# Kernel tuning notes

Measured on AMD Instinct MI355X. Metric: run time of the kernel, lower is better.

## Reference

```python
import jax, jax.numpy as jnp
import numpy as np

B, P, N, E, F, L = 64, 512, 512, 128, 512, 6
SQRT_E = 11.313708498984761
CLIP = 10.0
EPS = 1e-5

def _inorm(x, w, b):
    # InstanceNorm1d over node dim (axis=1) per (batch, channel); x: [B,N,E]
    mu = x.mean(axis=1, keepdims=True)
    var = x.var(axis=1, keepdims=True)
    return (x - mu) * jax.lax.rsqrt(var + EPS) * w + b

def setup_inputs():
    key = jax.random.key(0)
    ks = jax.random.split(key, 24)
    nrm = lambda k, shp, s=0.05: jax.random.normal(k, shp, dtype=jnp.float32) * s
    inp = {}
    inp['data'] = jax.random.uniform(ks[0], (B, N, 2), dtype=jnp.float32)
    inp['dist'] = -jax.random.uniform(ks[1], (B, N, N), dtype=jnp.float32)      # negative dist
    inp['cur_dist'] = -jax.random.uniform(ks[2], (B, P, N), dtype=jnp.float32)
    inp['capacity'] = jax.random.uniform(ks[3], (B, P), dtype=jnp.float32)
    inp['ninf_mask'] = jnp.zeros((B, P, N), jnp.float32)
    inp['log_scale'] = jnp.array([1.0], jnp.float32)
    # encoder params (Linear weights stored [in,out], i.e. torch weight transposed)
    inp['emb_W'] = nrm(ks[4], (2, E), 0.5); inp['emb_b'] = jnp.zeros((E,), jnp.float32)
    inp['Wq'] = nrm(ks[5], (L, E, E)); inp['Wk'] = nrm(ks[6], (L, E, E)); inp['Wv'] = nrm(ks[7], (L, E, E))
    inp['aft_alpha'] = jnp.ones((L,), jnp.float32)
    inp['n1_w'] = jnp.ones((L, E), jnp.float32); inp['n1_b'] = jnp.zeros((L, E), jnp.float32)
    inp['ff_W1'] = nrm(ks[8], (L, E, F)); inp['ff_b1'] = jnp.zeros((L, F), jnp.float32)
    inp['ff_W2'] = nrm(ks[9], (L, F, E)); inp['ff_b2'] = jnp.zeros((L, E), jnp.float32)
    inp['n2_w'] = jnp.ones((L, E), jnp.float32); inp['n2_b'] = jnp.zeros((L, E), jnp.float32)
    # decoder params
    inp['dWq'] = nrm(ks[10], (E + 1, E)); inp['dWk'] = nrm(ks[11], (E, E)); inp['dWv'] = nrm(ks[12], (E, E))
    inp['dec_aft_alpha'] = jnp.array([1.0], jnp.float32)
    inp['probs_alpha'] = jnp.array([1.0], jnp.float32)
    return inp

def reference(data, dist, cur_dist, capacity, ninf_mask, log_scale,
              emb_W, emb_b, Wq, Wk, Wv, aft_alpha, n1_w, n1_b,
              ff_W1, ff_b1, ff_W2, ff_b2, n2_w, n2_b,
              dWq, dWk, dWv, dec_aft_alpha, probs_alpha):
    ls = log_scale[0]
    # ---- encoder: stacked AFT layers ----
    x = data @ emb_W + emb_b                                   # [B,N,E]
    for l in range(L):
        q = x @ Wq[l]; k = x @ Wk[l]; v = x @ Wv[l]
        ad = jnp.exp(ls * aft_alpha[l] * dist)                 # [B,N,N]
        ek = jnp.exp(k)
        weighted = (ad @ (ek * v)) / (ad @ ek)                 # [B,N,E]
        out = jax.nn.sigmoid(q) * weighted
        h = _inorm(x + out, n1_w[l], n1_b[l])
        ff = jax.nn.relu(h @ ff_W1[l] + ff_b1[l]) @ ff_W2[l] + ff_b2[l]
        x = _inorm(h + ff, n2_w[l], n2_b[l])
    enc = x                                                    # [B,N,E]
    # ---- decoder ----
    k = enc @ dWk; v = enc @ dWv
    gmean = enc.mean(axis=1, keepdims=True)                    # [B,1,E]
    gmp = jnp.broadcast_to(gmean, (enc.shape[0], capacity.shape[1], enc.shape[2]))
    q = jnp.concatenate([gmp, capacity[:, :, None]], axis=2) @ dWq   # [B,P,E]
    ad = jnp.exp(ls * dec_aft_alpha[0] * cur_dist + ninf_mask)       # [B,P,N]
    ek = jnp.exp(k)
    weighted = (ad @ (ek * v)) / (ad @ ek)                     # [B,P,E]
    aft = jax.nn.sigmoid(q) * weighted
    score = jnp.einsum('bpe,bne->bpn', aft, enc) / SQRT_E
    score = score + ls * probs_alpha[0] * cur_dist
    score = CLIP * jnp.tanh(score) + ninf_mask
    return jax.nn.softmax(score, axis=2)                       # [B,P,N]
```

## Files before the change

### kernel.cpp

```cpp
#include <hip/hip_runtime.h>
#include <math.h>

#define B_ 64
#define N_ 512
#define P_ 512
#define E_ 128
#define F_ 512
#define L_ 6
#define SQRT_E_INV 0.08838834764831843f

typedef unsigned short u16;
typedef __attribute__((ext_vector_type(8))) short bf8;
typedef __attribute__((ext_vector_type(16))) float f16v;

__device__ inline u16 bf16r(float f) {
    unsigned u = __float_as_uint(f);
    u += 0x7fffu + ((u >> 16) & 1u);
    return (u16)(u >> 16);
}
__device__ inline float bf2f(u16 h) { return __uint_as_float((unsigned)h << 16); }

#define MFMA(a, b, c) __builtin_amdgcn_mfma_f32_32x32x16_bf16(a, b, c, 0, 0, 0)

struct Q3 {
    const u16 *A0, *A1;
    const u16 *qh, *ql, *vh, *vl, *kh, *kl;
    u16 *sq16, *y2t;
};

__launch_bounds__(256, 2) __global__ void qvk3_k(Q3 p)
{
    const int tid = threadIdx.x;
    const int lane = tid & 63, wv = tid >> 6;
    const int wm = wv & 1, wn = wv >> 1;
    const int ln = lane & 31, hk = lane >> 5;
    const int row0 = blockIdx.x * 64;

    __shared__ __align__(16) u16 As[2][64][40];
    __shared__ __align__(16) u16 Bs[6][128][40];

    f16v aq[2], av[2], ak[2];
#pragma unroll
    for (int nt = 0; nt < 2; ++nt)
#pragma unroll
        for (int q = 0; q < 16; ++q) { aq[nt][q] = 0.f; av[nt][q] = 0.f; ak[nt][q] = 0.f; }

    const int r = tid >> 2, kq = tid & 3;
    for (int k0 = 0; k0 < 128; k0 += 32) {
        size_t ga = (size_t)(row0 + r) * 128 + k0 + kq * 8;
        *(uint4*)&As[0][r][kq * 8] = *(const uint4*)(p.A0 + ga);
        *(uint4*)&As[1][r][kq * 8] = *(const uint4*)(p.A1 + ga);
#pragma unroll
        for (int i = 0; i < 2; ++i) {
            int s = tid + i * 256;
            int rb2 = s >> 2, q = s & 3;
            size_t gb = (size_t)rb2 * 128 + k0 + q * 8;
            *(uint4*)&Bs[0][rb2][q * 8] = *(const uint4*)(p.qh + gb);
            *(uint4*)&Bs[1][rb2][q * 8] = *(const uint4*)(p.ql + gb);
            *(uint4*)&Bs[2][rb2][q * 8] = *(const uint4*)(p.vh + gb);
            *(uint4*)&Bs[3][rb2][q * 8] = *(const uint4*)(p.vl + gb);
            *(uint4*)&Bs[4][rb2][q * 8] = *(const uint4*)(p.kh + gb);
            *(uint4*)&Bs[5][rb2][q * 8] = *(const uint4*)(p.kl + gb);
        }
        __syncthreads();
#pragma unroll
        for (int s = 0; s < 2; ++s) {
            bf8 ah = *(const bf8*)&As[0][wm * 32 + ln][s * 16 + hk * 8];
            bf8 al = *(const bf8*)&As[1][wm * 32 + ln][s * 16 + hk * 8];
#pragma unroll
            for (int nt = 0; nt < 2; ++nt) {
                const int br = wn * 64 + nt * 32 + ln, sc = s * 16 + hk * 8;
                bf8 bqh = *(const bf8*)&Bs[0][br][sc];
                bf8 bql = *(const bf8*)&Bs[1][br][sc];
                bf8 bvh = *(const bf8*)&Bs[2][br][sc];
                bf8 bvl = *(const bf8*)&Bs[3][br][sc];
                bf8 bkh = *(const bf8*)&Bs[4][br][sc];
                bf8 bkl = *(const bf8*)&Bs[5][br][sc];
                aq[nt] = MFMA(ah, bqh, aq[nt]);
                aq[nt] = MFMA(ah, bql, aq[nt]);
                aq[nt] = MFMA(al, bqh, aq[nt]);
                av[nt] = MFMA(ah, bvh, av[nt]);
                av[nt] = MFMA(ah, bvl, av[nt]);
                av[nt] = MFMA(al, bvh, av[nt]);
                ak[nt] = MFMA(ah, bkh, ak[nt]);
                ak[nt] = MFMA(ah, bkl, ak[nt]);
                ak[nt] = MFMA(al, bkh, ak[nt]);
            }
        }
        __syncthreads();
    }

#pragma unroll
    for (int nt = 0; nt < 2; ++nt) {
        int gn = wn * 64 + nt * 32 + ln;
#pragma unroll
        for (int g = 0; g < 4; ++g) {
            int rb = row0 + wm * 32 + g * 8 + hk * 4;
            int bb = rb >> 9, nb = rb & 511;
            u16 pe[4], pv[4];
#pragma unroll
            for (int rr = 0; rr < 4; ++rr) {
                float vq = aq[nt][g * 4 + rr];
                p.sq16[(size_t)(rb + rr) * 128 + gn] =
                    bf16r(1.f / (1.f + __expf(-vq)));
                u16 hv = bf16r(av[nt][g * 4 + rr]);
                u16 he = bf16r(__expf(ak[nt][g * 4 + rr]));
                pe[rr] = he;
                pv[rr] = bf16r(bf2f(hv) * bf2f(he));
            }
            uint2 ue, uv;
            ue.x = pe[0] | ((unsigned)pe[1] << 16);
            ue.y = pe[2] | ((unsigned)pe[3] << 16);
            uv.x = pv[0] | ((unsigned)pv[1] << 16);
            uv.y = pv[2] | ((unsigned)pv[3] << 16);
            *(uint2*)(p.y2t + (size_t)bb * 131072 + (size_t)gn * 512 + nb) = uv;
            *(uint2*)(p.y2t + (size_t)bb * 131072 + (size_t)(128 + gn) * 512 + nb) = ue;
        }
    }
}

struct QV {
    const u16 *A0, *A1;
    const u16 *vh, *vl, *kh, *kl;
    u16* y2t;
};

__launch_bounds__(256, 3) __global__ void qvk_vk_k(QV p)
{
    const int tid = threadIdx.x;
    const int lane = tid & 63, wv = tid >> 6;
    const int wm = wv & 1, wn = wv >> 1;
    const int ln = lane & 31, hk = lane >> 5;
    const int row0 = blockIdx.x * 64;

    __shared__ __align__(16) u16 As[2][64][40];
    __shared__ __align__(16) u16 Bs[4][128][40];

    f16v av[2], ak[2];
#pragma unroll
    for (int nt = 0; nt < 2; ++nt)
#pragma unroll
        for (int q = 0; q < 16; ++q) { av[nt][q] = 0.f; ak[nt][q] = 0.f; }

    const int r = tid >> 2, kq = tid & 3;
    for (int k0 = 0; k0 < 128; k0 += 32) {
        size_t ga = (size_t)(row0 + r) * 128 + k0 + kq * 8;
        *(uint4*)&As[0][r][kq * 8] = *(const uint4*)(p.A0 + ga);
        *(uint4*)&As[1][r][kq * 8] = *(const uint4*)(p.A1 + ga);
#pragma unroll
        for (int i = 0; i < 2; ++i) {
            int s = tid + i * 256;
            int rb2 = s >> 2, q = s & 3;
            size_t gb = (size_t)rb2 * 128 + k0 + q * 8;
            *(uint4*)&Bs[0][rb2][q * 8] = *(const uint4*)(p.vh + gb);
            *(uint4*)&Bs[1][rb2][q * 8] = *(const uint4*)(p.vl + gb);
            *(uint4*)&Bs[2][rb2][q * 8] = *(const uint4*)(p.kh + gb);
            *(uint4*)&Bs[3][rb2][q * 8] = *(const uint4*)(p.kl + gb);
        }
        __syncthreads();
#pragma unroll
        for (int s = 0; s < 2; ++s) {
            bf8 ah = *(const bf8*)&As[0][wm * 32 + ln][s * 16 + hk * 8];
            bf8 al = *(const bf8*)&As[1][wm * 32 + ln][s * 16 + hk * 8];
#pragma unroll
            for (int nt = 0; nt < 2; ++nt) {
                const int br = wn * 64 + nt * 32 + ln, sc = s * 16 + hk * 8;
                bf8 bvh = *(const bf8*)&Bs[0][br][sc];
                bf8 bvl = *(const bf8*)&Bs[1][br][sc];
                bf8 bkh = *(const bf8*)&Bs[2][br][sc];
                bf8 bkl = *(const bf8*)&Bs[3][br][sc];
                av[nt] = MFMA(ah, bvh, av[nt]);
                av[nt] = MFMA(ah, bvl, av[nt]);
                av[nt] = MFMA(al, bvh, av[nt]);
                ak[nt] = MFMA(ah, bkh, ak[nt]);
                ak[nt] = MFMA(ah, bkl, ak[nt]);
                ak[nt] = MFMA(al, bkh, ak[nt]);
            }
        }
        __syncthreads();
    }

#pragma unroll
    for (int nt = 0; nt < 2; ++nt) {
        int gn = wn * 64 + nt * 32 + ln;
#pragma unroll
        for (int g = 0; g < 4; ++g) {
            int rb = row0 + wm * 32 + g * 8 + hk * 4;
            int bb = rb >> 9, nb = rb & 511;
            u16 pe[4], pv[4];
#pragma unroll
            for (int rr = 0; rr < 4; ++rr) {
                u16 hv = bf16r(av[nt][g * 4 + rr]);
                u16 he = bf16r(__expf(ak[nt][g * 4 + rr]));
                pe[rr] = he;
                pv[rr] = bf16r(bf2f(hv) * bf2f(he));
            }
            uint2 ue, uv;
            ue.x = pe[0] | ((unsigned)pe[1] << 16);
            ue.y = pe[2] | ((unsigned)pe[3] << 16);
            uv.x = pv[0] | ((unsigned)pv[1] << 16);
            uv.y = pv[2] | ((unsigned)pv[3] << 16);
            *(uint2*)(p.y2t + (size_t)bb * 131072 + (size_t)gn * 512 + nb) = uv;
            *(uint2*)(p.y2t + (size_t)bb * 131072 + (size_t)(128 + gn) * 512 + nb) = ue;
        }
    }
}

struct AP2 {
    const float *A0, *A1;
    const u16 *B0, *sq;
    u16 *gh, *gl;
    const float *s1, *s2; int s2i;
};

template <int OPA, int SG>
__launch_bounds__(256, 3) __global__ void aft2_k(AP2 p)
{
    const int tid = threadIdx.x;
    const int lane = tid & 63, wv = tid >> 6;
    const int wm = wv & 1, wn = wv >> 1;
    const int ln = lane & 31, hk = lane >> 5;

    const int id = blockIdx.x;
    const int xcd = id & 7, slot = id >> 3;
    const int bz = xcd * 8 + (slot >> 3);
    const int row0 = (slot & 7) * 64;

    __shared__ __align__(16) u16 As[2][64][40];
    __shared__ __align__(16) u16 Bs[2][256][40];

    f16v acc[4];
#pragma unroll
    for (int j = 0; j < 4; ++j)
#pragma unroll
        for (int q = 0; q < 16; ++q) acc[j][q] = 0.f;

    const float ascale = p.s1[0] * p.s2[p.s2i];
    const float* Af = p.A0 + (size_t)bz * 262144 + (size_t)row0 * 512;
    const float* Mf = (OPA == 2)
        ? (p.A1 + (size_t)bz * 262144 + (size_t)row0 * 512) : (const float*)0;
    const u16* Bb = p.B0 + (size_t)bz * 131072;

    const int r = tid >> 2, kq = tid & 3;
    float fa[8], fm[8];
    uint4 vb[4];

#define AFT_LOAD(K0)                                                          \
    {                                                                         \
        size_t ga = (size_t)r * 512 + (K0) + kq * 8;                          \
        *(float4*)&fa[0] = *(const float4*)(Af + ga);                         \
        *(float4*)&fa[4] = *(const float4*)(Af + ga + 4);                     \
        if (OPA == 2) {                                                       \
            *(float4*)&fm[0] = *(const float4*)(Mf + ga);                     \
            *(float4*)&fm[4] = *(const float4*)(Mf + ga + 4);                 \
        }                                                                     \
        size_t gb = (size_t)tid * 512 + (K0);                                 \
        _Pragma("unroll") for (int q = 0; q < 4; ++q)                         \
            vb[q] = *(const uint4*)(Bb + gb + q * 8);                         \
    }

#define AFT_WRITE(BUF)                                                        \
    {                                                                         \
        float f[8];                                                           \
        _Pragma("unroll") for (int j = 0; j < 8; ++j) {                       \
            float t = (OPA == 2) ? fmaf(ascale, fa[j], fm[j]) : ascale * fa[j]; \
            f[j] = __expf(t);                                                 \
        }                                                                     \
        uint4 pk;                                                             \
        pk.x = bf16r(f[0]) | ((unsigned)bf16r(f[1]) << 16);                   \
        pk.y = bf16r(f[2]) | ((unsigned)bf16r(f[3]) << 16);                   \
        pk.z = bf16r(f[4]) | ((unsigned)bf16r(f[5]) << 16);                   \
        pk.w = bf16r(f[6]) | ((unsigned)bf16r(f[7]) << 16);                   \
        *(uint4*)&As[BUF][r][kq * 8] = pk;                                    \
        _Pragma("unroll") for (int q = 0; q < 4; ++q)                         \
            *(uint4*)&Bs[BUF][tid][q * 8] = vb[q];                            \
    }

#define AFT_COMPUTE(BUF)                                                      \
    {                                                                         \
        _Pragma("unroll") for (int s = 0; s < 2; ++s) {                       \
            bf8 ah = *(const bf8*)&As[BUF][wm * 32 + ln][s * 16 + hk * 8];    \
            _Pragma("unroll") for (int j = 0; j < 4; ++j) {                   \
                int br = ((j >> 1) << 7) + wn * 64 + ((j & 1) << 5) + ln;     \
                bf8 bh = *(const bf8*)&Bs[BUF][br][s * 16 + hk * 8];          \
                acc[j] = MFMA(ah, bh, acc[j]);                                \
            }                                                                 \
        }                                                                     \
    }

    AFT_LOAD(0);
    AFT_WRITE(0);
    __syncthreads();

    int cur = 0;
    for (int k0 = 32; k0 < 512; k0 += 32) {
        AFT_LOAD(k0);
        AFT_COMPUTE(cur);
        AFT_WRITE(cur ^ 1);
        __syncthreads();
        cur ^= 1;
    }
    AFT_COMPUTE(cur);

#undef AFT_LOAD
#undef AFT_WRITE
#undef AFT_COMPUTE

    const u16* sqb = SG ? (p.sq + (size_t)bz * 65536) : (const u16*)0;
    u16* ghb = p.gh + (size_t)bz * 65536;
    u16* glb = p.gl + (size_t)bz * 65536;
#pragma unroll
    for (int j = 0; j < 2; ++j) {
        int e = wn * 64 + j * 32 + ln;
#pragma unroll
        for (int g = 0; g < 4; ++g) {
#pragma unroll
            for (int rr = 0; rr < 4; ++rr) {
                int row = row0 + wm * 32 + g * 8 + hk * 4 + rr;
                float num = acc[j][g * 4 + rr];
                float den = acc[j + 2][g * 4 + rr];
                float pv = num / den;
                if (SG) pv *= bf2f(sqb[(size_t)row * 128 + e]);
                u16 hi = bf16r(pv);
                ghb[(size_t)row * 128 + e] = hi;
                glb[(size_t)row * 128 + e] = bf16r(pv - bf2f(hi));
            }
        }
    }
}

struct F12 {
    const u16 *A0, *A1;
    const u16 *w1h, *w1l;
    const u16 *w2h, *w2l;
    const float *b1, *b2;
    float* of;
};

__launch_bounds__(512, 2) __global__ void ffn12_k(F12 p)
{
    const int tid = threadIdx.x;
    const int lane = tid & 63, wv = tid >> 6;
    const int wm = wv & 1, wn = wv >> 1;
    const int ln = lane & 31, hk = lane >> 5;
    const int row0 = blockIdx.x * 64;

    __shared__ __align__(16) u16 Bs[2][128][136];
    __shared__ __align__(16) u16 ff1c[4][64][136];

    bf8 ar0[8], ar1[8];
    {
        const size_t arow = (size_t)(row0 + wm * 32 + ln) * 128;
#pragma unroll
        for (int s = 0; s < 8; ++s) {
            ar0[s] = *(const bf8*)(p.A0 + arow + s * 16 + hk * 8);
            ar1[s] = *(const bf8*)(p.A1 + arow + s * 16 + hk * 8);
        }
    }

    const int lcol = wn * 32 + ln;

    for (int ct = 0; ct < 4; ++ct) {
#pragma unroll
        for (int i = 0; i < 4; ++i) {
            int idx = tid + i * 512;
            int col = idx >> 4, q = idx & 15;
            size_t gb = (size_t)(ct * 128 + col) * 128 + q * 8;
            *(uint4*)&Bs[0][col][q * 8] = *(const uint4*)(p.w1h + gb);
            *(uint4*)&Bs[1][col][q * 8] = *(const uint4*)(p.w1l + gb);
        }
        __syncthreads();

        f16v a0, a1, a2;
#pragma unroll
        for (int q = 0; q < 16; ++q) { a0[q] = 0.f; a1[q] = 0.f; a2[q] = 0.f; }
#pragma unroll
        for (int s = 0; s < 8; ++s) {
            bf8 bh = *(const bf8*)&Bs[0][lcol][s * 16 + hk * 8];
            bf8 bl = *(const bf8*)&Bs[1][lcol][s * 16 + hk * 8];
            a0 = MFMA(ar0[s], bh, a0);
            a1 = MFMA(ar0[s], bl, a1);
            a2 = MFMA(ar1[s], bh, a2);
        }
        __syncthreads();

        float bv = p.b1[ct * 128 + lcol];
#pragma unroll
        for (int g = 0; g < 4; ++g) {
#pragma unroll
            for (int rr = 0; rr < 4; ++rr) {
                int lr = wm * 32 + g * 8 + hk * 4 + rr;
                float v = a0[g * 4 + rr] + a1[g * 4 + rr] + a2[g * 4 + rr] + bv;
                ff1c[ct][lr][lcol] = bf16r(fmaxf(v, 0.f));
            }
        }
    }
    __syncthreads();

    f16v c0, c1;
#pragma unroll
    for (int q = 0; q < 16; ++q) { c0[q] = 0.f; c1[q] = 0.f; }
    for (int kc = 0; kc < 4; ++kc) {
#pragma unroll
        for (int i = 0; i < 4; ++i) {
            int idx = tid + i * 512;
            int col = idx >> 4, q = idx & 15;
            size_t gb = (size_t)col * 512 + kc * 128 + q * 8;
            *(uint4*)&Bs[0][col][q * 8] = *(const uint4*)(p.w2h + gb);
            *(uint4*)&Bs[1][col][q * 8] = *(const uint4*)(p.w2l + gb);
        }
        __syncthreads();
#pragma unroll
        for (int s = 0; s < 8; ++s) {
            bf8 af = *(const bf8*)&ff1c[kc][wm * 32 + ln][s * 16 + hk * 8];
            bf8 bh = *(const bf8*)&Bs[0][lcol][s * 16 + hk * 8];
            bf8 bl = *(const bf8*)&Bs[1][lcol][s * 16 + hk * 8];
            c0 = MFMA(af, bh, c0);
            c1 = MFMA(af, bl, c1);
        }
        __syncthreads();
    }

    float bv = p.b2[lcol];
#pragma unroll
    for (int g = 0; g < 4; ++g) {
#pragma unroll
        for (int rr = 0; rr < 4; ++rr) {
            int rb = row0 + wm * 32 + g * 8 + hk * 4 + rr;
            p.of[(size_t)rb * 128 + lcol] = c0[g * 4 + rr] + c1[g * 4 + rr] + bv;
        }
    }
}

struct SP2 {
    const u16 *A0, *A1, *B0, *B1;
    float* out;
    const float *cd, *cm;
    const float *s1, *s2;
};

__launch_bounds__(256, 2) __global__ void score_sm_k(SP2 p)
{
    const int tid = threadIdx.x;
    const int lane = tid & 63, wv = tid >> 6;
    const int wm = wv & 1, wn = wv >> 1;
    const int ln = lane & 31, hk = lane >> 5;

    const int id = blockIdx.x;
    const int xcd = id & 7, s_ = id >> 3;
    const int bz = xcd * 8 + (s_ & 7);
    const int row0 = (s_ >> 3) * 64;

    __shared__ __align__(16) u16 As[2][64][136];
    __shared__ __align__(16) u16 Bs[2][128][72];
    __shared__ float rs[2][64];

#pragma unroll
    for (int i = 0; i < 8; ++i) {
        int idx = tid + i * 256;
        int pl = idx >> 10, rem = idx & 1023;
        int row = rem >> 4, q = rem & 15;
        const u16* src = pl ? p.A1 : p.A0;
        *(uint4*)&As[pl][row][q * 8] =
            *(const uint4*)(src + ((size_t)bz * 512 + row0 + row) * 128 + q * 8);
    }

    const float sp = p.s1[0] * p.s2[0];
    f16v accs[4][2];
    float rsum[16];
#pragma unroll
    for (int i = 0; i < 16; ++i) rsum[i] = 0.f;

#pragma unroll
    for (int ct = 0; ct < 4; ++ct) {
#pragma unroll
        for (int nt = 0; nt < 2; ++nt)
#pragma unroll
            for (int q = 0; q < 16; ++q) accs[ct][nt][q] = 0.f;

        for (int kc = 0; kc < 128; kc += 64) {
#pragma unroll
            for (int i = 0; i < 8; ++i) {
                int idx = tid + i * 256;
                int pl = idx >> 10, rem = idx & 1023;
                int row = rem >> 3, q = rem & 7;
                const u16* src = pl ? p.B1 : p.B0;
                *(uint4*)&Bs[pl][row][q * 8] =
                    *(const uint4*)(src + ((size_t)bz * 512 + ct * 128 + row) * 128
                                    + kc + q * 8);
            }
            __syncthreads();
#pragma unroll
            for (int s = 0; s < 4; ++s) {
                bf8 ah = *(const bf8*)&As[0][wm * 32 + ln][kc + s * 16 + hk * 8];
                bf8 al = *(const bf8*)&As[1][wm * 32 + ln][kc + s * 16 + hk * 8];
#pragma unroll
                for (int nt = 0; nt < 2; ++nt) {
                    bf8 bh = *(const bf8*)&Bs[0][wn * 64 + nt * 32 + ln][s * 16 + hk * 8];
                    bf8 bl = *(const bf8*)&Bs[1][wn * 64 + nt * 32 + ln][s * 16 + hk * 8];
                    accs[ct][nt] = MFMA(ah, bh, accs[ct][nt]);
                    accs[ct][nt] = MFMA(ah, bl, accs[ct][nt]);
                    accs[ct][nt] = MFMA(al, bh, accs[ct][nt]);
                }
            }
            __syncthreads();
        }

#pragma unroll
        for (int nt = 0; nt < 2; ++nt) {
            int gn = ct * 128 + wn * 64 + nt * 32 + ln;
#pragma unroll
            for (int g = 0; g < 4; ++g) {
#pragma unroll
                for (int rr = 0; rr < 4; ++rr) {
                    int grow = row0 + wm * 32 + g * 8 + hk * 4 + rr;
                    size_t ix = (size_t)bz * 262144 + (size_t)grow * 512 + gn;
                    float sc = fmaf(accs[ct][nt][g * 4 + rr], SQRT_E_INV,
                                    sp * p.cd[ix]);
                    float e2 = __expf(2.f * sc);
                    float th = 1.f - 2.f / (e2 + 1.f);
                    float ev = __expf(10.f * th + p.cm[ix]);
                    accs[ct][nt][g * 4 + rr] = ev;
                    rsum[g * 4 + rr] += ev;
                }
            }
        }
    }

#pragma unroll
    for (int i = 0; i < 16; ++i) {
#pragma unroll
        for (int o = 1; o < 32; o <<= 1) rsum[i] += __shfl_xor(rsum[i], o);
    }
    __syncthreads();
    if (ln == 0) {
#pragma unroll
        for (int i = 0; i < 16; ++i) {
            int lr = wm * 32 + (i >> 2) * 8 + hk * 4 + (i & 3);
            rs[wn][lr] = rsum[i];
        }
    }
    __syncthreads();
    float invr[16];
#pragma unroll
    for (int i = 0; i < 16; ++i) {
        int lr = wm * 32 + (i >> 2) * 8 + hk * 4 + (i & 3);
        invr[i] = 1.f / (rs[0][lr] + rs[1][lr]);
    }

#pragma unroll
    for (int ct = 0; ct < 4; ++ct)
#pragma unroll
        for (int nt = 0; nt < 2; ++nt) {
            int gn = ct * 128 + wn * 64 + nt * 32 + ln;
#pragma unroll
            for (int g = 0; g < 4; ++g)
#pragma unroll
                for (int rr = 0; rr < 4; ++rr) {
                    int grow = row0 + wm * 32 + g * 8 + hk * 4 + rr;
                    size_t ix = (size_t)bz * 262144 + (size_t)grow * 512 + gn;
                    p.out[ix] = accs[ct][nt][g * 4 + rr] * invr[g * 4 + rr];
                }
        }
}

template <int MODE>
__launch_bounds__(256) __global__ void inorm_k(
    const u16* __restrict__ ah, const u16* __restrict__ al,
    const u16* __restrict__ g0, const u16* __restrict__ g1,
    const float* __restrict__ f1,
    const float* __restrict__ nw, const float* __restrict__ nbv,
    u16* __restrict__ oh, u16* __restrict__ ol)
{
    const int bb = blockIdx.x, e0 = blockIdx.y * 16;
    const int tid = threadIdx.x, el = tid & 3, no = tid >> 2;
    const size_t base = (size_t)bb * N_ * E_ + e0 + el * 4;

    float4 vals[8];
    float s1x = 0, s1y = 0, s1z = 0, s1w = 0;
    float s2x = 0, s2y = 0, s2z = 0, s2w = 0;
#pragma unroll
    for (int i = 0; i < 8; ++i) {
        int n = no * 8 + i;
        size_t ad = base + (size_t)n * E_;
        uint2 h2 = *(const uint2*)(ah + ad);
        uint2 l2 = *(const uint2*)(al + ad);
        float x0 = bf2f((u16)h2.x) + bf2f((u16)l2.x);
        float x1 = bf2f((u16)(h2.x >> 16)) + bf2f((u16)(l2.x >> 16));
        float x2 = bf2f((u16)h2.y) + bf2f((u16)l2.y);
        float x3 = bf2f((u16)(h2.y >> 16)) + bf2f((u16)(l2.y >> 16));
        float4 v;
        if (MODE == 1) {
            uint2 a2 = *(const uint2*)(g0 + ad);
            uint2 b2 = *(const uint2*)(g1 + ad);
            v.x = x0 + bf2f((u16)a2.x) + bf2f((u16)b2.x);
            v.y = x1 + bf2f((u16)(a2.x >> 16)) + bf2f((u16)(b2.x >> 16));
            v.z = x2 + bf2f((u16)a2.y) + bf2f((u16)b2.y);
            v.w = x3 + bf2f((u16)(a2.y >> 16)) + bf2f((u16)(b2.y >> 16));
        } else {
            float4 ff = *(const float4*)(f1 + ad);
            v.x = x0 + ff.x; v.y = x1 + ff.y; v.z = x2 + ff.z; v.w = x3 + ff.w;
        }
        vals[i] = v;
        s1x += v.x; s1y += v.y; s1z += v.z; s1w += v.w;
        s2x = fmaf(v.x, v.x, s2x); s2y = fmaf(v.y, v.y, s2y);
        s2z = fmaf(v.z, v.z, s2z); s2w = fmaf(v.w, v.w, s2w);
    }

    __shared__ float4 r1[256], r2[256];
    r1[tid] = make_float4(s1x, s1y, s1z, s1w);
    r2[tid] = make_float4(s2x, s2y, s2z, s2w);
    __syncthreads();
    for (int s = 128; s >= 4; s >>= 1) {
        if (tid < s) {
            float4 u = r1[tid], w = r1[tid + s];
            r1[tid] = make_float4(u.x + w.x, u.y + w.y, u.z + w.z, u.w + w.w);
            float4 pq = r2[tid], q = r2[tid + s];
            r2[tid] = make_float4(pq.x + q.x, pq.y + q.y, pq.z + q.z, pq.w + q.w);
        }
        __syncthreads();
    }
    __shared__ float4 mu_s[4], rs_s[4];
    if (tid < 4) {
        float4 m = r1[tid], q = r2[tid];
        m.x *= (1.f / N_); m.y *= (1.f / N_); m.z *= (1.f / N_); m.w *= (1.f / N_);
        q.x *= (1.f / N_); q.y *= (1.f / N_); q.z *= (1.f / N_); q.w *= (1.f / N_);
        float4 rsq;
        rsq.x = rsqrtf(q.x - m.x * m.x + 1e-5f);
        rsq.y = rsqrtf(q.y - m.y * m.y + 1e-5f);
        rsq.z = rsqrtf(q.z - m.z * m.z + 1e-5f);
        rsq.w = rsqrtf(q.w - m.w * m.w + 1e-5f);
        mu_s[tid] = m; rs_s[tid] = rsq;
    }
    __syncthreads();
    float4 mu = mu_s[el], rsq = rs_s[el];
    float4 w4 = *(const float4*)(nw + e0 + el * 4);
    float4 b4 = *(const float4*)(nbv + e0 + el * 4);
#pragma unroll
    for (int i = 0; i < 8; ++i) {
        size_t ad = base + (size_t)(no * 8 + i) * E_;
        float4 v = vals[i];
        v.x = fmaf((v.x - mu.x) * rsq.x, w4.x, b4.x);
        v.y = fmaf((v.y - mu.y) * rsq.y, w4.y, b4.y);
        v.z = fmaf((v.z - mu.z) * rsq.z, w4.z, b4.z);
        v.w = fmaf((v.w - mu.w) * rsq.w, w4.w, b4.w);
        u16 h0 = bf16r(v.x), h1 = bf16r(v.y), h2v = bf16r(v.z), h3 = bf16r(v.w);
        u16 l0 = bf16r(v.x - bf2f(h0)), l1 = bf16r(v.y - bf2f(h1));
        u16 l2v = bf16r(v.z - bf2f(h2v)), l3 = bf16r(v.w - bf2f(h3));
        uint2 ph, pl;
        ph.x = h0 | ((unsigned)h1 << 16); ph.y = h2v | ((unsigned)h3 << 16);
        pl.x = l0 | ((unsigned)l1 << 16); pl.y = l2v | ((unsigned)l3 << 16);
        *(uint2*)(oh + ad) = ph;
        *(uint2*)(ol + ad) = pl;
    }
}

__global__ void wprep_k(const float* __restrict__ W, u16* __restrict__ Th,
                        u16* __restrict__ Tl, int K, int N)
{
    const int z = blockIdx.z;
    const float* Wz = W + (size_t)z * K * N;
    u16* Hh = Th + (size_t)z * K * N;
    u16* Hl = Tl + (size_t)z * K * N;
    __shared__ float t[32][33];
    const int j = threadIdx.x & 31, i0 = threadIdx.x >> 5;
    const int k0 = blockIdx.x * 32, n0 = blockIdx.y * 32;
    for (int i = i0; i < 32; i += 8)
        t[i][j] = Wz[(size_t)(k0 + i) * N + n0 + j];
    __syncthreads();
    for (int i = i0; i < 32; i += 8) {
        float v = t[j][i];
        u16 h = bf16r(v);
        u16 l = bf16r(v - bf2f(h));
        size_t o = (size_t)(n0 + i) * K + k0 + j;
        Hh[o] = h; Hl[o] = l;
    }
}

__global__ void embed_k(const float* __restrict__ data, const float* __restrict__ W,
                        const float* __restrict__ bias,
                        u16* __restrict__ xh, u16* __restrict__ xl)
{
    size_t idx = (size_t)blockIdx.x * 256 + threadIdx.x;
    int e = idx & 127;
    size_t bn = idx >> 7;
    float v = fmaf(data[bn * 2], W[e], fmaf(data[bn * 2 + 1], W[128 + e], bias[e]));
    u16 h = bf16r(v);
    xh[idx] = h;
    xl[idx] = bf16r(v - bf2f(h));
}

__launch_bounds__(512) __global__
void gq_k(const u16* __restrict__ xh, const u16* __restrict__ xl,
          const float* __restrict__ dWq, float* __restrict__ gq)
{
    int b = blockIdx.x;
    int tid = threadIdx.x;
    int e = tid & 127, qd = tid >> 7;
    float s = 0.f;
    for (int n = qd; n < N_; n += 4) {
        size_t ix = ((size_t)b * N_ + n) * E_ + e;
        s += bf2f(xh[ix]) + bf2f(xl[ix]);
    }
    __shared__ float part[512];
    __shared__ float gm[128];
    part[tid] = s;
    __syncthreads();
    if (tid < 128)
        gm[tid] = (part[tid] + part[tid + 128] + part[tid + 256] + part[tid + 384]) *
                  (1.f / N_);
    __syncthreads();
    if (tid < 128) {
        float acc = 0.f;
        for (int kk = 0; kk < 128; ++kk) acc = fmaf(gm[kk], dWq[kk * 128 + tid], acc);
        gq[b * 128 + tid] = acc;
    }
}

__global__ void dec_aft_k(const float* __restrict__ gq, const float* __restrict__ cap,
                          const float* __restrict__ dWq,
                          const u16* __restrict__ rh, const u16* __restrict__ rl,
                          u16* __restrict__ oh, u16* __restrict__ ol)
{
    size_t idx = (size_t)blockIdx.x * 256 + threadIdx.x;
    int e = idx & 127;
    size_t bp = idx >> 7;
    int b = (int)(bp >> 9);
    float q = fmaf(cap[bp], dWq[128 * 128 + e], gq[b * 128 + e]);
    float sg = 1.f / (1.f + __expf(-q));
    float v = sg * (bf2f(rh[idx]) + bf2f(rl[idx]));
    u16 h = bf16r(v);
    oh[idx] = h;
    ol[idx] = bf16r(v - bf2f(h));
}

extern "C" void kernel_launch(void* const* d_in, const int* in_sizes, int n_in,
                              void* d_out, int out_size, void* d_ws, size_t ws_size,
                              hipStream_t stream)
{
    const float* data      = (const float*)d_in[0];
    const float* dist      = (const float*)d_in[1];
    const float* cur_dist  = (const float*)d_in[2];
    const float* capacity  = (const float*)d_in[3];
    const float* ninf      = (const float*)d_in[4];
    const float* log_scale = (const float*)d_in[5];
    const float* emb_W     = (const float*)d_in[6];
    const float* emb_b     = (const float*)d_in[7];
    const float* Wq        = (const float*)d_in[8];
    const float* Wk        = (const float*)d_in[9];
    const float* Wv        = (const float*)d_in[10];
    const float* aft_alpha = (const float*)d_in[11];
    const float* n1_w      = (const float*)d_in[12];
    const float* n1_b      = (const float*)d_in[13];
    const float* ffW1      = (const float*)d_in[14];
    const float* ffb1      = (const float*)d_in[15];
    const float* ffW2      = (const float*)d_in[16];
    const float* ffb2      = (const float*)d_in[17];
    const float* n2_w      = (const float*)d_in[18];
    const float* n2_b      = (const float*)d_in[19];
    const float* dWq       = (const float*)d_in[20];
    const float* dWk       = (const float*)d_in[21];
    const float* dWv       = (const float*)d_in[22];
    const float* dec_alpha = (const float*)d_in[23];
    const float* p_alpha   = (const float*)d_in[24];
    float* out = (float*)d_out;

    char* W = (char*)d_ws;
    size_t off = 0;
    auto take = [&](size_t n) { void* pp = W + off; off += (n + 255) & ~(size_t)255; return pp; };
    const size_t SZP = (size_t)B_ * N_ * E_ * 2;

    u16* xh   = (u16*)take(SZP);
    u16* xl   = (u16*)take(SZP);
    u16* hh   = (u16*)take(SZP);
    u16* hl   = (u16*)take(SZP);
    u16* sq16 = (u16*)take(SZP);
    u16* gh   = (u16*)take(SZP);
    u16* gl   = (u16*)take(SZP);
    u16* y2t  = (u16*)take(2 * SZP);
    float* ff2 = (float*)take((size_t)B_ * N_ * E_ * 4);
    u16* wqt_h = (u16*)take(196608); u16* wqt_l = (u16*)take(196608);
    u16* wkt_h = (u16*)take(196608); u16* wkt_l = (u16*)take(196608);
    u16* wvt_h = (u16*)take(196608); u16* wvt_l = (u16*)take(196608);
    u16* w1t_h = (u16*)take(786432); u16* w1t_l = (u16*)take(786432);
    u16* w2t_h = (u16*)take(786432); u16* w2t_l = (u16*)take(786432);
    u16* dkt_h = (u16*)take(32768);  u16* dkt_l = (u16*)take(32768);
    u16* dvt_h = (u16*)take(32768);  u16* dvt_l = (u16*)take(32768);
    float* gq = (float*)take(32768);
    if (ws_size < off) return;

    wprep_k<<<dim3(4, 4, 6), 256, 0, stream>>>(Wq, wqt_h, wqt_l, 128, 128);
    wprep_k<<<dim3(4, 4, 6), 256, 0, stream>>>(Wk, wkt_h, wkt_l, 128, 128);
    wprep_k<<<dim3(4, 4, 6), 256, 0, stream>>>(Wv, wvt_h, wvt_l, 128, 128);
    wprep_k<<<dim3(4, 16, 6), 256, 0, stream>>>(ffW1, w1t_h, w1t_l, 128, 512);
    wprep_k<<<dim3(16, 4, 6), 256, 0, stream>>>(ffW2, w2t_h, w2t_l, 512, 128);
    wprep_k<<<dim3(4, 4, 1), 256, 0, stream>>>(dWk, dkt_h, dkt_l, 128, 128);
    wprep_k<<<dim3(4, 4, 1), 256, 0, stream>>>(dWv, dvt_h, dvt_l, 128, 128);

    embed_k<<<16384, 256, 0, stream>>>(data, emb_W, emb_b, xh, xl);

    for (int l = 0; l < L_; ++l) {
        Q3 q3{};
        q3.A0 = xh; q3.A1 = xl;
        q3.qh = wqt_h + l * 16384; q3.ql = wqt_l + l * 16384;
        q3.vh = wvt_h + l * 16384; q3.vl = wvt_l + l * 16384;
        q3.kh = wkt_h + l * 16384; q3.kl = wkt_l + l * 16384;
        q3.sq16 = sq16; q3.y2t = y2t;
        qvk3_k<<<512, 256, 0, stream>>>(q3);

        AP2 ap{};
        ap.A0 = dist; ap.B0 = y2t; ap.sq = sq16; ap.gh = gh; ap.gl = gl;
        ap.s1 = log_scale; ap.s2 = aft_alpha; ap.s2i = l;
        aft2_k<1, 1><<<512, 256, 0, stream>>>(ap);

        inorm_k<1><<<dim3(B_, 8), 256, 0, stream>>>(
            xh, xl, gh, gl, nullptr, n1_w + l * 128, n1_b + l * 128, hh, hl);

        F12 f12{};
        f12.A0 = hh; f12.A1 = hl;
        f12.w1h = w1t_h + l * 65536; f12.w1l = w1t_l + l * 65536;
        f12.w2h = w2t_h + l * 65536; f12.w2l = w2t_l + l * 65536;
        f12.b1 = ffb1 + l * 512; f12.b2 = ffb2 + l * 128;
        f12.of = ff2;
        ffn12_k<<<512, 512, 0, stream>>>(f12);

        inorm_k<2><<<dim3(B_, 8), 256, 0, stream>>>(
            hh, hl, nullptr, nullptr, ff2, n2_w + l * 128, n2_b + l * 128, xh, xl);
    }

    {
        QV qv{};
        qv.A0 = xh; qv.A1 = xl;
        qv.vh = dvt_h; qv.vl = dvt_l;
        qv.kh = dkt_h; qv.kl = dkt_l;
        qv.y2t = y2t;
        qvk_vk_k<<<512, 256, 0, stream>>>(qv);
        gq_k<<<B_, 512, 0, stream>>>(xh, xl, dWq, gq);

        AP2 ap{};
        ap.A0 = cur_dist; ap.A1 = ninf; ap.B0 = y2t; ap.gh = gh; ap.gl = gl;
        ap.s1 = log_scale; ap.s2 = dec_alpha; ap.s2i = 0;
        aft2_k<2, 0><<<512, 256, 0, stream>>>(ap);

        dec_aft_k<<<16384, 256, 0, stream>>>(gq, capacity, dWq, gh, gl, hh, hl);

        SP2 sp{};
        sp.A0 = hh; sp.A1 = hl; sp.B0 = xh; sp.B1 = xl;
        sp.out = out; sp.cd = cur_dist; sp.cm = ninf;
        sp.s1 = log_scale; sp.s2 = p_alpha;
        score_sm_k<<<512, 256, 0, stream>>>(sp);
    }
}
```

Before: 1.198 ms.

## Pre-convert dist to bf16, pipeline FFN weight loads, widen score kernel

Converts the fp32 dist matrix to bf16 once before the layer loop so the six AFT passes read half the bytes, and pre-fuses cur_dist*scale+mask into bf16 for the decoder AFT. Rewrites the FFN kernel to double-buffer 64-wide weight chunks in shared memory, overlapping global loads with MFMA work. Reworks score_sm_k to 512 threads with one n-tile per wave and prefetches the cur_dist and mask values before the matmul. Rounding the dist and mask inputs to bf16 before exp reduces precision, and the prep kernels add extra passes over memory.

```diff
diff --git a/kernel.cpp b/kernel.cpp
--- a/kernel.cpp
+++ b/kernel.cpp
@@ -207,7 +207,7 @@
 }
 
 struct AP2 {
-    const float *A0, *A1;
+    const u16 *A16;
     const u16 *B0, *sq;
     u16 *gh, *gl;
     const float *s1, *s2; int s2i;
@@ -235,25 +235,17 @@
 #pragma unroll
         for (int q = 0; q < 16; ++q) acc[j][q] = 0.f;
 
-    const float ascale = p.s1[0] * p.s2[p.s2i];
-    const float* Af = p.A0 + (size_t)bz * 262144 + (size_t)row0 * 512;
-    const float* Mf = (OPA == 2)
-        ? (p.A1 + (size_t)bz * 262144 + (size_t)row0 * 512) : (const float*)0;
+    const float ascale = (OPA == 1) ? p.s1[0] * p.s2[p.s2i] : 0.f;
+    const u16* Af = p.A16 + (size_t)bz * 262144 + (size_t)row0 * 512;
     const u16* Bb = p.B0 + (size_t)bz * 131072;
 
     const int r = tid >> 2, kq = tid & 3;
-    float fa[8], fm[8];
+    uint4 va;
     uint4 vb[4];
 
 #define AFT_LOAD(K0)                                                          \
     {                                                                         \
-        size_t ga = (size_t)r * 512 + (K0) + kq * 8;                          \
-        *(float4*)&fa[0] = *(const float4*)(Af + ga);                         \
-        *(float4*)&fa[4] = *(const float4*)(Af + ga + 4);                     \
-        if (OPA == 2) {                                                       \
-            *(float4*)&fm[0] = *(const float4*)(Mf + ga);                     \
-            *(float4*)&fm[4] = *(const float4*)(Mf + ga + 4);                 \
-        }                                                                     \
+        va = *(const uint4*)(Af + (size_t)r * 512 + (K0) + kq * 8);           \
         size_t gb = (size_t)tid * 512 + (K0);                                 \
         _Pragma("unroll") for (int q = 0; q < 4; ++q)                         \
             vb[q] = *(const uint4*)(Bb + gb + q * 8);                         \
@@ -261,9 +253,12 @@
 
 #define AFT_WRITE(BUF)                                                        \
     {                                                                         \
+        u16 a8[8];                                                            \
+        *(uint4*)a8 = va;                                                     \
         float f[8];                                                           \
         _Pragma("unroll") for (int j = 0; j < 8; ++j) {                       \
-            float t = (OPA == 2) ? fmaf(ascale, fa[j], fm[j]) : ascale * fa[j]; \
+            float t = bf2f(a8[j]);                                            \
+            if (OPA == 1) t *= ascale;                                        \
             f[j] = __expf(t);                                                 \
         }                                                                     \
         uint4 pk;                                                             \
@@ -345,7 +340,7 @@
     const int ln = lane & 31, hk = lane >> 5;
     const int row0 = blockIdx.x * 64;
 
-    __shared__ __align__(16) u16 Bs[2][128][136];
+    __shared__ __align__(16) u16 Ws[2][2][128][72];
     __shared__ __align__(16) u16 ff1c[4][64][136];
 
     bf8 ar0[8], ar1[8];
@@ -359,77 +354,112 @@
     }
 
     const int lcol = wn * 32 + ln;
-
-    for (int ct = 0; ct < 4; ++ct) {
-#pragma unroll
-        for (int i = 0; i < 4; ++i) {
-            int idx = tid + i * 512;
-            int col = idx >> 4, q = idx & 15;
-            size_t gb = (size_t)(ct * 128 + col) * 128 + q * 8;
-            *(uint4*)&Bs[0][col][q * 8] = *(const uint4*)(p.w1h + gb);
-            *(uint4*)&Bs[1][col][q * 8] = *(const uint4*)(p.w1l + gb);
-        }
+    const int sc_ = tid >> 3, sq_ = tid & 7;
+    uint4 wr[2][2];
+
+#define F_LOAD1(CT, KC)                                                       \
+    {                                                                         \
+        _Pragma("unroll") for (int pl = 0; pl < 2; ++pl) {                    \
+            const u16* src = pl ? p.w1l : p.w1h;                              \
+            _Pragma("unroll") for (int it = 0; it < 2; ++it) {                \
+                int c = sc_ + it * 64;                                        \
+                wr[pl][it] = *(const uint4*)(src +                            \
+                    (size_t)((CT) * 128 + c) * 128 + (KC) * 64 + sq_ * 8);    \
+            }                                                                 \
+        }                                                                     \
+    }
+
+#define F_LOAD2(J)                                                            \
+    {                                                                         \
+        _Pragma("unroll") for (int pl = 0; pl < 2; ++pl) {                    \
+            const u16* src = pl ? p.w2l : p.w2h;                              \
+            _Pragma("unroll") for (int it = 0; it < 2; ++it) {                \
+                int c = sc_ + it * 64;                                        \
+                wr[pl][it] = *(const uint4*)(src +                            \
+                    (size_t)c * 512 + (J) * 64 + sq_ * 8);                    \
+            }                                                                 \
+        }                                                                     \
+    }
+
+#define F_STORE(BUF)                                                          \
+    {                                                                         \
+        _Pragma("unroll") for (int pl = 0; pl < 2; ++pl)                      \
+            _Pragma("unroll") for (int it = 0; it < 2; ++it)                  \
+                *(uint4*)&Ws[BUF][pl][sc_ + it * 64][sq_ * 8] = wr[pl][it];   \
+    }
+
+    F_LOAD1(0, 0);
+    F_STORE(0);
+    __syncthreads();
+    int buf = 0;
+    f16v a0, a1, a2;
+#pragma unroll
+    for (int st = 0; st < 8; ++st) {
+        const int ct = st >> 1, kc = st & 1;
+        if (st < 7) { F_LOAD1((st + 1) >> 1, (st + 1) & 1); }
+        else        { F_LOAD2(0); }
+        if (kc == 0) {
+#pragma unroll
+            for (int q = 0; q < 16; ++q) { a0[q] = 0.f; a1[q] = 0.f; a2[q] = 0.f; }
+        }
+#pragma unroll
+        for (int s = 0; s < 4; ++s) {
+            bf8 bh = *(const bf8*)&Ws[buf][0][lcol][s * 16 + hk * 8];
+            bf8 bl = *(const bf8*)&Ws[buf][1][lcol][s * 16 + hk * 8];
+            a0 = MFMA(ar0[kc * 4 + s], bh, a0);
+            a1 = MFMA(ar0[kc * 4 + s], bl, a1);
+            a2 = MFMA(ar1[kc * 4 + s], bh, a2);
+        }
+        if (kc == 1) {
+            float bv = p.b1[ct * 128 + lcol];
+#pragma unroll
+            for (int g = 0; g < 4; ++g)
+#pragma unroll
+                for (int rr = 0; rr < 4; ++rr) {
+                    int lr = wm * 32 + g * 8 + hk * 4 + rr;
+                    float v = a0[g * 4 + rr] + a1[g * 4 + rr] + a2[g * 4 + rr] + bv;
+                    ff1c[ct][lr][lcol] = bf16r(fmaxf(v, 0.f));
+                }
+        }
+        F_STORE(buf ^ 1);
         __syncthreads();
-
-        f16v a0, a1, a2;
-#pragma unroll
-        for (int q = 0; q < 16; ++q) { a0[q] = 0.f; a1[q] = 0.f; a2[q] = 0.f; }
-#pragma unroll
-        for (int s = 0; s < 8; ++s) {
-            bf8 bh = *(const bf8*)&Bs[0][lcol][s * 16 + hk * 8];
-            bf8 bl = *(const bf8*)&Bs[1][lcol][s * 16 + hk * 8];
-            a0 = MFMA(ar0[s], bh, a0);
-            a1 = MFMA(ar0[s], bl, a1);
-            a2 = MFMA(ar1[s], bh, a2);
-        }
-        __syncthreads();
-
-        float bv = p.b1[ct * 128 + lcol];
-#pragma unroll
-        for (int g = 0; g < 4; ++g) {
-#pragma unroll
-            for (int rr = 0; rr < 4; ++rr) {
-                int lr = wm * 32 + g * 8 + hk * 4 + rr;
-                float v = a0[g * 4 + rr] + a1[g * 4 + rr] + a2[g * 4 + rr] + bv;
-                ff1c[ct][lr][lcol] = bf16r(fmaxf(v, 0.f));
-            }
-        }
-    }
-    __syncthreads();
+        buf ^= 1;
+    }
 
     f16v c0, c1;
 #pragma unroll
     for (int q = 0; q < 16; ++q) { c0[q] = 0.f; c1[q] = 0.f; }
-    for (int kc = 0; kc < 4; ++kc) {
-#pragma unroll
-        for (int i = 0; i < 4; ++i) {
-            int idx = tid + i * 512;
-            int col = idx >> 4, q = idx & 15;
-            size_t gb = (size_t)col * 512 + kc * 128 + q * 8;
-            *(uint4*)&Bs[0][col][q * 8] = *(const uint4*)(p.w2h + gb);
-            *(uint4*)&Bs[1][col][q * 8] = *(const uint4*)(p.w2l + gb);
-        }
-        __syncthreads();
-#pragma unroll
-        for (int s = 0; s < 8; ++s) {
-            bf8 af = *(const bf8*)&ff1c[kc][wm * 32 + ln][s * 16 + hk * 8];
-            bf8 bh = *(const bf8*)&Bs[0][lcol][s * 16 + hk * 8];
-            bf8 bl = *(const bf8*)&Bs[1][lcol][s * 16 + hk * 8];
+#pragma unroll
+    for (int j = 0; j < 8; ++j) {
+        if (j < 7) F_LOAD2(j + 1);
+#pragma unroll
+        for (int s = 0; s < 4; ++s) {
+            bf8 af = *(const bf8*)&ff1c[j >> 1][wm * 32 + ln]
+                                      [(j & 1) * 64 + s * 16 + hk * 8];
+            bf8 bh = *(const bf8*)&Ws[buf][0][lcol][s * 16 + hk * 8];
+            bf8 bl = *(const bf8*)&Ws[buf][1][lcol][s * 16 + hk * 8];
             c0 = MFMA(af, bh, c0);
             c1 = MFMA(af, bl, c1);
         }
-        __syncthreads();
-    }
+        if (j < 7) {
+            F_STORE(buf ^ 1);
+            __syncthreads();
+            buf ^= 1;
+        }
+    }
+
+#undef F_LOAD1
+#undef F_LOAD2
+#undef F_STORE
 
     float bv = p.b2[lcol];
 #pragma unroll
-    for (int g = 0; g < 4; ++g) {
+    for (int g = 0; g < 4; ++g)
 #pragma unroll
         for (int rr = 0; rr < 4; ++rr) {
             int rb = row0 + wm * 32 + g * 8 + hk * 4 + rr;
             p.of[(size_t)rb * 128 + lcol] = c0[g * 4 + rr] + c1[g * 4 + rr] + bv;
         }
-    }
 }
 
 struct SP2 {
@@ -439,7 +469,7 @@
     const float *s1, *s2;
 };
 
-__launch_bounds__(256, 2) __global__ void score_sm_k(SP2 p)
+__launch_bounds__(512, 4) __global__ void score_sm_k(SP2 p)
 {
     const int tid = threadIdx.x;
     const int lane = tid & 63, wv = tid >> 6;
@@ -453,11 +483,11 @@
 
     __shared__ __align__(16) u16 As[2][64][136];
     __shared__ __align__(16) u16 Bs[2][128][72];
-    __shared__ float rs[2][64];
-
-#pragma unroll
-    for (int i = 0; i < 8; ++i) {
-        int idx = tid + i * 256;
+    __shared__ float rs[4][64];
+
+#pragma unroll
+    for (int i = 0; i < 4; ++i) {
+        int idx = tid + i * 512;
         int pl = idx >> 10, rem = idx & 1023;
         int row = rem >> 4, q = rem & 15;
         const u16* src = pl ? p.A1 : p.A0;
@@ -466,22 +496,30 @@
     }
 
     const float sp = p.s1[0] * p.s2[0];
-    f16v accs[4][2];
-    float rsum[16];
-#pragma unroll
-    for (int i = 0; i < 16; ++i) rsum[i] = 0.f;
+    f16v accs[4];
 
 #pragma unroll
     for (int ct = 0; ct < 4; ++ct) {
-#pragma unroll
-        for (int nt = 0; nt < 2; ++nt)
-#pragma unroll
-            for (int q = 0; q < 16; ++q) accs[ct][nt][q] = 0.f;
-
-        for (int kc = 0; kc < 128; kc += 64) {
-#pragma unroll
-            for (int i = 0; i < 8; ++i) {
-                int idx = tid + i * 256;
+        const int gn = ct * 128 + wn * 32 + ln;
+        float cdv[16], cmv[16];
+#pragma unroll
+        for (int g = 0; g < 4; ++g)
+#pragma unroll
+            for (int rr = 0; rr < 4; ++rr) {
+                int grow = row0 + wm * 32 + g * 8 + hk * 4 + rr;
+                size_t ix = (size_t)bz * 262144 + (size_t)grow * 512 + gn;
+                cdv[g * 4 + rr] = p.cd[ix];
+                cmv[g * 4 + rr] = p.cm[ix];
+            }
+#pragma unroll
+        for (int q = 0; q < 16; ++q) accs[ct][q] = 0.f;
+
+#pragma unroll
+        for (int kh = 0; kh < 2; ++kh) {
+            const int kc = kh * 64;
+#pragma unroll
+            for (int i = 0; i < 4; ++i) {
+                int idx = tid + i * 512;
                 int pl = idx >> 10, rem = idx & 1023;
                 int row = rem >> 3, q = rem & 7;
                 const u16* src = pl ? p.B1 : p.B0;
@@ -494,39 +532,28 @@
             for (int s = 0; s < 4; ++s) {
                 bf8 ah = *(const bf8*)&As[0][wm * 32 + ln][kc + s * 16 + hk * 8];
                 bf8 al = *(const bf8*)&As[1][wm * 32 + ln][kc + s * 16 + hk * 8];
-#pragma unroll
-                for (int nt = 0; nt < 2; ++nt) {
-                    bf8 bh = *(const bf8*)&Bs[0][wn * 64 + nt * 32 + ln][s * 16 + hk * 8];
-                    bf8 bl = *(const bf8*)&Bs[1][wn * 64 + nt * 32 + ln][s * 16 + hk * 8];
-                    accs[ct][nt] = MFMA(ah, bh, accs[ct][nt]);
-                    accs[ct][nt] = MFMA(ah, bl, accs[ct][nt]);
-                    accs[ct][nt] = MFMA(al, bh, accs[ct][nt]);
-                }
+                bf8 bh = *(const bf8*)&Bs[0][wn * 32 + ln][s * 16 + hk * 8];
+                bf8 bl = *(const bf8*)&Bs[1][wn * 32 + ln][s * 16 + hk * 8];
+                accs[ct] = MFMA(ah, bh, accs[ct]);
+                accs[ct] = MFMA(ah, bl, accs[ct]);
+                accs[ct] = MFMA(al, bh, accs[ct]);
             }
             __syncthreads();
         }
 
 #pragma unroll
-        for (int nt = 0; nt < 2; ++nt) {
-            int gn = ct * 128 + wn * 64 + nt * 32 + ln;
-#pragma unroll
-            for (int g = 0; g < 4; ++g) {
-#pragma unroll
-                for (int rr = 0; rr < 4; ++rr) {
-                    int grow = row0 + wm * 32 + g * 8 + hk * 4 + rr;
-                    size_t ix = (size_t)bz * 262144 + (size_t)grow * 512 + gn;
-                    float sc = fmaf(accs[ct][nt][g * 4 + rr], SQRT_E_INV,
-                                    sp * p.cd[ix]);
-                    float e2 = __expf(2.f * sc);
-                    float th = 1.f - 2.f / (e2 + 1.f);
-                    float ev = __expf(10.f * th + p.cm[ix]);
-                    accs[ct][nt][g * 4 + rr] = ev;
-                    rsum[g * 4 + rr] += ev;
-                }
-            }
-        }
-    }
-
+        for (int i = 0; i < 16; ++i) {
+            float sc = fmaf(accs[ct][i], SQRT_E_INV, sp * cdv[i]);
+            float e2 = __expf(2.f * sc);
+            float th = 1.f - 2.f / (e2 + 1.f);
+            accs[ct][i] = __expf(10.f * th + cmv[i]);
+        }
+    }
+
+    float rsum[16];
+#pragma unroll
+    for (int i = 0; i < 16; ++i)
+        rsum[i] = accs[0][i] + accs[1][i] + accs[2][i] + accs[3][i];
 #pragma unroll
     for (int i = 0; i < 16; ++i) {
 #pragma unroll
@@ -545,23 +572,21 @@
 #pragma unroll
     for (int i = 0; i < 16; ++i) {
         int lr = wm * 32 + (i >> 2) * 8 + hk * 4 + (i & 3);
-        invr[i] = 1.f / (rs[0][lr] + rs[1][lr]);
-    }
-
-#pragma unroll
-    for (int ct = 0; ct < 4; ++ct)
-#pragma unroll
-        for (int nt = 0; nt < 2; ++nt) {
-            int gn = ct * 128 + wn * 64 + nt * 32 + ln;
-#pragma unroll
-            for (int g = 0; g < 4; ++g)
-#pragma unroll
-                for (int rr = 0; rr < 4; ++rr) {
-                    int grow = row0 + wm * 32 + g * 8 + hk * 4 + rr;
-                    size_t ix = (size_t)bz * 262144 + (size_t)grow * 512 + gn;
-                    p.out[ix] = accs[ct][nt][g * 4 + rr] * invr[g * 4 + rr];
-                }
-        }
+        invr[i] = 1.f / (rs[0][lr] + rs[1][lr] + rs[2][lr] + rs[3][lr]);
+    }
+
+#pragma unroll
+    for (int ct = 0; ct < 4; ++ct) {
+        int gn = ct * 128 + wn * 32 + ln;
+#pragma unroll
+        for (int g = 0; g < 4; ++g)
+#pragma unroll
+            for (int rr = 0; rr < 4; ++rr) {
+                int grow = row0 + wm * 32 + g * 8 + hk * 4 + rr;
+                size_t ix = (size_t)bz * 262144 + (size_t)grow * 512 + gn;
+                p.out[ix] = accs[ct][g * 4 + rr] * invr[g * 4 + rr];
+            }
+    }
 }
 
 template <int MODE>
@@ -675,6 +700,37 @@
         size_t o = (size_t)(n0 + i) * K + k0 + j;
         Hh[o] = h; Hl[o] = l;
     }
+}
+
+__global__ void distprep_k(const float* __restrict__ src, u16* __restrict__ dst)
+{
+    size_t i = ((size_t)blockIdx.x * 256 + threadIdx.x) * 8;
+    float4 f0 = *(const float4*)(src + i);
+    float4 f1 = *(const float4*)(src + i + 4);
+    uint4 pk;
+    pk.x = bf16r(f0.x) | ((unsigned)bf16r(f0.y) << 16);
+    pk.y = bf16r(f0.z) | ((unsigned)bf16r(f0.w) << 16);
+    pk.z = bf16r(f1.x) | ((unsigned)bf16r(f1.y) << 16);
+    pk.w = bf16r(f1.z) | ((unsigned)bf16r(f1.w) << 16);
+    *(uint4*)(dst + i) = pk;
+}
+
+__global__ void decprep_k(const float* __restrict__ cd, const float* __restrict__ nf,
+                          const float* __restrict__ s1, const float* __restrict__ s2,
+                          u16* __restrict__ dst)
+{
+    const float da = s1[0] * s2[0];
+    size_t i = ((size_t)blockIdx.x * 256 + threadIdx.x) * 8;
+    float4 c0 = *(const float4*)(cd + i);
+    float4 c1 = *(const float4*)(cd + i + 4);
+    float4 m0 = *(const float4*)(nf + i);
+    float4 m1 = *(const float4*)(nf + i + 4);
+    uint4 pk;
+    pk.x = bf16r(fmaf(da, c0.x, m0.x)) | ((unsigned)bf16r(fmaf(da, c0.y, m0.y)) << 16);
+    pk.y = bf16r(fmaf(da, c0.z, m0.z)) | ((unsigned)bf16r(fmaf(da, c0.w, m0.w)) << 16);
+    pk.z = bf16r(fmaf(da, c1.x, m1.x)) | ((unsigned)bf16r(fmaf(da, c1.y, m1.y)) << 16);
+    pk.w = bf16r(fmaf(da, c1.z, m1.z)) | ((unsigned)bf16r(fmaf(da, c1.w, m1.w)) << 16);
+    *(uint4*)(dst + i) = pk;
 }
 
 __global__ void embed_k(const float* __restrict__ data, const float* __restrict__ W,
@@ -779,6 +835,7 @@
     u16* gl   = (u16*)take(SZP);
     u16* y2t  = (u16*)take(2 * SZP);
     float* ff2 = (float*)take((size_t)B_ * N_ * E_ * 4);
+    u16* d16  = (u16*)take((size_t)B_ * N_ * N_ * 2);
     u16* wqt_h = (u16*)take(196608); u16* wqt_l = (u16*)take(196608);
     u16* wkt_h = (u16*)take(196608); u16* wkt_l = (u16*)take(196608);
     u16* wvt_h = (u16*)take(196608); u16* wvt_l = (u16*)take(196608);
@@ -789,6 +846,8 @@
     float* gq = (float*)take(32768);
     if (ws_size < off) return;
 
+    u16* am16 = d16;
+
     wprep_k<<<dim3(4, 4, 6), 256, 0, stream>>>(Wq, wqt_h, wqt_l, 128, 128);
     wprep_k<<<dim3(4, 4, 6), 256, 0, stream>>>(Wk, wkt_h, wkt_l, 128, 128);
     wprep_k<<<dim3(4, 4, 6), 256, 0, stream>>>(Wv, wvt_h, wvt_l, 128, 128);
@@ -797,6 +856,7 @@
     wprep_k<<<dim3(4, 4, 1), 256, 0, stream>>>(dWk, dkt_h, dkt_l, 128, 128);
     wprep_k<<<dim3(4, 4, 1), 256, 0, stream>>>(dWv, dvt_h, dvt_l, 128, 128);
 
+    distprep_k<<<8192, 256, 0, stream>>>(dist, d16);
     embed_k<<<16384, 256, 0, stream>>>(data, emb_W, emb_b, xh, xl);
 
     for (int l = 0; l < L_; ++l) {
@@ -809,7 +869,7 @@
         qvk3_k<<<512, 256, 0, stream>>>(q3);
 
         AP2 ap{};
-        ap.A0 = dist; ap.B0 = y2t; ap.sq = sq16; ap.gh = gh; ap.gl = gl;
+        ap.A16 = d16; ap.B0 = y2t; ap.sq = sq16; ap.gh = gh; ap.gl = gl;
         ap.s1 = log_scale; ap.s2 = aft_alpha; ap.s2i = l;
         aft2_k<1, 1><<<512, 256, 0, stream>>>(ap);
 
@@ -837,10 +897,12 @@
         qvk_vk_k<<<512, 256, 0, stream>>>(qv);
         gq_k<<<B_, 512, 0, stream>>>(xh, xl, dWq, gq);
 
+        decprep_k<<<8192, 256, 0, stream>>>(cur_dist, ninf, log_scale, dec_alpha, am16);
+
         AP2 ap{};
-        ap.A0 = cur_dist; ap.A1 = ninf; ap.B0 = y2t; ap.gh = gh; ap.gl = gl;
+        ap.A16 = am16; ap.B0 = y2t; ap.gh = gh; ap.gl = gl;
         ap.s1 = log_scale; ap.s2 = dec_alpha; ap.s2i = 0;
-        aft2_k<2, 0><<<512, 256, 0, stream>>>(ap);
+        aft2_k<3, 0><<<512, 256, 0, stream>>>(ap);
 
         dec_aft_k<<<16384, 256, 0, stream>>>(gq, capacity, dWq, gh, gl, hh, hl);
 
@@ -848,6 +910,6 @@
         sp.A0 = hh; sp.A1 = hl; sp.B0 = xh; sp.B1 = xl;
         sp.out = out; sp.cd = cur_dist; sp.cm = ninf;
         sp.s1 = log_scale; sp.s2 = p_alpha;
-        score_sm_k<<<512, 256, 0, stream>>>(sp);
-    }
-}
+        score_sm_k<<<512, 512, 0, stream>>>(sp);
+    }
+}
```

New measurement: 1.131 ms. 5.5% less time.
